# Optimization experiments

Hardware: AMD Instinct MI355X
Metric: run time of the kernel (lower is better)

## Reference

```python
import jax, jax.numpy as jnp
import numpy as np

EPS = 1e-8


def setup_inputs() -> dict:
    key = jax.random.key(0)
    ks = jax.random.split(key, 5)
    B, C, F, T = 2, 8, 1024, 256
    Ch, Fh = 4 * C, 4 * F  # expanded channels/features
    s_pw1 = 1.0 / np.sqrt(F)
    s_dw1 = 1.0 / np.sqrt(C)
    s_pw2 = 1.0 / np.sqrt(Fh)
    s_dw2 = 1.0 / np.sqrt(Ch)
    return {
        "x": jax.random.normal(ks[0], (B, C, F, T), jnp.float32),
        "ln_w": jnp.ones((C, F), jnp.float32),
        "ln_b": jnp.zeros((C, F), jnp.float32),
        "pw1": jax.random.uniform(ks[1], (C, Fh, F), jnp.float32, -s_pw1, s_pw1),
        "dw1": jax.random.uniform(ks[2], (Ch, C), jnp.float32, -s_dw1, s_dw1),
        "pw2": jax.random.uniform(ks[3], (Ch, F, Fh), jnp.float32, -s_pw2, s_pw2),
        "dw2": jax.random.uniform(ks[4], (C, Ch), jnp.float32, -s_dw2, s_dw2),
    }


def _mc_layernorm(x, w, b):
    # x: (B,C,F,T); normalize over feature axis (2), affine per (channel, feature)
    mu = jnp.mean(x, axis=2, keepdims=True)
    var = jnp.var(x, axis=2, keepdims=True)
    xn = (x - mu) * jax.lax.rsqrt(var + EPS)
    return xn * w[None, :, :, None] + b[None, :, :, None]


def reference(x, ln_w, ln_b, pw1, dw1, pw2, dw2):
    h = _mc_layernorm(x, ln_w, ln_b)
    # per-channel positionwise linear: (C, F_out, F_in)
    h = jnp.einsum('bcft,cgf->bcgt', h, pw1)
    # channel mixing (depthwise linear across channels): (C_out, C_in)
    h = jnp.einsum('bcft,dc->bdft', h, dw1)
    h = jnp.square(jax.nn.relu(h))  # squared ReLU
    h = jnp.einsum('bcft,cgf->bcgt', h, pw2)
    h = jnp.einsum('bcft,dc->bdft', h, dw2)
    return x + h
```

## Files before the change

kernel.cpp:

```cpp
#include <hip/hip_runtime.h>

#define B_DIM  2
#define C_DIM  8
#define F_DIM  1024
#define T_DIM  256
#define CH_DIM 32
#define FH_DIM 4096
#define BT_DIM 512

typedef __bf16 bf16x8 __attribute__((ext_vector_type(8)));
typedef __bf16 bf16x4 __attribute__((ext_vector_type(4)));
typedef float  f32x4  __attribute__((ext_vector_type(4)));

__device__ __forceinline__ void async16(const void* g, void* l) {
  __builtin_amdgcn_global_load_lds(
      (const __attribute__((address_space(1))) unsigned int*)g,
      (__attribute__((address_space(3))) unsigned int*)l, 16, 0, 0);
}

#define LGKM0_SCHED() do { \
    asm volatile("s_waitcnt lgkmcnt(0)" ::: "memory"); \
    __builtin_amdgcn_sched_barrier(0); } while (0)

__global__ void ln_kernel(const float* __restrict__ x,
                          const float* __restrict__ lnw,
                          const float* __restrict__ lnb,
                          __bf16* __restrict__ hn) {
  const int tb = blockIdx.x;
  const int c  = blockIdx.y;
  const int b  = blockIdx.z;
  const int tid = threadIdx.x;
  const int tx = tid & 15, ty = tid >> 4;
  const int t0 = tb * 16;

  const float* xp = x + (size_t)(b * C_DIM + c) * F_DIM * T_DIM;

  float s = 0.f, s2 = 0.f;
  for (int f = ty; f < F_DIM; f += 16) {
    float v = xp[f * T_DIM + t0 + tx];
    s += v; s2 += v * v;
  }
  __shared__ float ps[16][16], ps2[16][16];
  __shared__ float mean_s[16], rstd_s[16];
  ps[ty][tx] = s; ps2[ty][tx] = s2;
  __syncthreads();
  if (tid < 16) {
    float a = 0.f, a2 = 0.f;
    for (int j = 0; j < 16; ++j) { a += ps[j][tid]; a2 += ps2[j][tid]; }
    float mu  = a * (1.0f / F_DIM);
    float var = a2 * (1.0f / F_DIM) - mu * mu;
    mean_s[tid] = mu;
    rstd_s[tid] = rsqrtf(var + 1e-8f);
  }
  __syncthreads();

  __shared__ float tile[64][17];
  __bf16* hp = hn + ((size_t)c * BT_DIM + b * T_DIM + t0) * F_DIM;
  for (int ff = 0; ff < 16; ++ff) {
    const int f0 = ff * 64;
#pragma unroll
    for (int it = 0; it < 4; ++it) {
      int e  = it * 256 + tid;
      int fi = e >> 4, ti = e & 15;
      float v = xp[(f0 + fi) * T_DIM + t0 + ti];
      v = (v - mean_s[ti]) * rstd_s[ti];
      v = v * lnw[c * F_DIM + f0 + fi] + lnb[c * F_DIM + f0 + fi];
      tile[fi][ti] = v;
    }
    __syncthreads();
#pragma unroll
    for (int it = 0; it < 4; ++it) {
      int e  = it * 256 + tid;
      int fx = e & 63, tw = e >> 6;
      hp[(size_t)tw * F_DIM + f0 + fx] = (__bf16)tile[fx][tw];
    }
    __syncthreads();
  }
}

template<int TPB_BITS, bool CT>
__global__ __launch_bounds__(512, 2)
void gemm_8p(const float* __restrict__ A, const __bf16* __restrict__ Bm,
             __bf16* __restrict__ Co, const int M, const int K) {
  const int NT = K >> 6;
  const int bid = blockIdx.x;
  const int xcd = bid & 7, idx = bid >> 3;
  const int batch = xcd * (32 >> TPB_BITS) + (idx >> TPB_BITS);
  const int tile  = idx & ((1 << TPB_BITS) - 1);
  const int mt = tile >> 1, nt = tile & 1;

  const int tid = threadIdx.x, lane = tid & 63, wid = tid >> 6;

  const float*  Ab = A  + (size_t)batch * M * K + (size_t)(mt * 256) * K;
  const __bf16* Bb = Bm + (size_t)batch * BT_DIM * K + (size_t)(nt * 256) * K;

  extern __shared__ __align__(16) char smem[];
  __bf16* const AS = (__bf16*)smem;
  __bf16* const BS = (__bf16*)(smem + 65536);

  const int wm = wid >> 2, wn = wid & 3;
  const int lr = lane & 15, khi = lane >> 4;
  const int lsw = lr & 7;

  const int b_row = lane >> 3;
  const int b_src = (lane & 7) ^ b_row;

  f32x4 acc[8][4] = {};
  float4 sa[8];
  bf16x8 af[4];

  auto issueB1 = [&](int sbuf, int tt, int j) {
    const int chunk = j * 8 + wid;
    async16(Bb + (size_t)(chunk * 8 + b_row) * K + (size_t)tt * 64 + b_src * 8,
            BS + sbuf * 16384 + chunk * 512);
  };
  auto issueA2 = [&](int tt, int i0) {
#pragma unroll
    for (int i = i0; i < i0 + 2; ++i) {
      const int c = i * 512 + tid;
      sa[i] = *(const float4*)(Ab + (size_t)(c >> 4) * K + (size_t)tt * 64 + (c & 15) * 4);
    }
  };
  auto writeA2 = [&](int abuf, int i0) {
#pragma unroll
    for (int i = i0; i < i0 + 2; ++i) {
      const int c = i * 512 + tid;
      const int r = c >> 4;
      const int s = ((c & 15) >> 1) ^ (r & 7);
      bf16x4 v;
      v[0]=(__bf16)sa[i].x; v[1]=(__bf16)sa[i].y; v[2]=(__bf16)sa[i].z; v[3]=(__bf16)sa[i].w;
      *(bf16x4*)(AS + abuf * 16384 + r * 64 + s * 8 + (c & 1) * 4) = v;
    }
  };
  auto readA = [&](int abuf, int mq, int ks) {
#pragma unroll
    for (int j = 0; j < 4; ++j) {
      const int row = wm * 128 + (mq * 4 + j) * 16 + lr;
      af[j] = *(const bf16x8*)(AS + abuf * 16384 + row * 64 + (((ks << 2) | khi) ^ lsw) * 8);
    }
  };
  auto readB2 = [&](bf16x8* bq, int rbuf, int np, int ks) {
#pragma unroll
    for (int j = 0; j < 2; ++j) {
      const int row = wn * 64 + (np * 2 + j) * 16 + lr;
      bq[j] = *(const bf16x8*)(BS + rbuf * 16384 + row * 64 + (((ks << 2) | khi) ^ lsw) * 8);
    }
  };
  auto mfma8 = [&](const bf16x8* bq, int mq, int np) {
    __builtin_amdgcn_s_setprio(1);
#pragma unroll
    for (int j = 0; j < 4; ++j)
#pragma unroll
      for (int n = 0; n < 2; ++n)
        acc[mq * 4 + j][np * 2 + n] =
            __builtin_amdgcn_mfma_f32_16x16x32_bf16(af[j], bq[n], acc[mq * 4 + j][np * 2 + n], 0, 0, 0);
    __builtin_amdgcn_s_setprio(0);
  };

  issueA2(0, 0); issueA2(0, 2); issueA2(0, 4); issueA2(0, 6);
  issueB1(0, 0, 0); issueB1(0, 0, 1); issueB1(0, 0, 2); issueB1(0, 0, 3);
  issueB1(1, 1, 0); issueB1(1, 1, 1); issueB1(1, 1, 2); issueB1(1, 1, 3);
  writeA2(0, 0); writeA2(0, 2); writeA2(0, 4); writeA2(0, 6);
  issueA2(1, 0); issueA2(1, 2); issueA2(1, 4); issueA2(1, 6);
  asm volatile("s_waitcnt vmcnt(12)" ::: "memory");
  LGKM0_SCHED();
  __builtin_amdgcn_s_barrier();

  int cur = 0;
  for (int t = 0; t < NT; ++t) {
    const int rd = t % 3, st = (t + 2) % 3;
    const int tN = (t + 2 < NT) ? t + 2 : NT - 1;
    bf16x8 bq[2];
    issueB1(st, tN, 0);
    readA(cur, 0, 0); readB2(bq, rd, 0, 0);
    __builtin_amdgcn_s_barrier(); LGKM0_SCHED();
    mfma8(bq, 0, 0); __builtin_amdgcn_s_barrier();
    issueB1(st, tN, 1);
    readB2(bq, rd, 1, 0);
    __builtin_amdgcn_s_barrier(); LGKM0_SCHED();
    mfma8(bq, 0, 1); __builtin_amdgcn_s_barrier();
    issueB1(st, tN, 2);
    readA(cur, 1, 0); readB2(bq, rd, 0, 0);
    __builtin_amdgcn_s_barrier(); LGKM0_SCHED();
    mfma8(bq, 1, 0); __builtin_amdgcn_s_barrier();
    issueB1(st, tN, 3);
    readB2(bq, rd, 1, 0);
    __builtin_amdgcn_s_barrier(); LGKM0_SCHED();
    mfma8(bq, 1, 1); __builtin_amdgcn_s_barrier();
    writeA2(cur ^ 1, 0); issueA2(tN, 0);
    readA(cur, 0, 1); readB2(bq, rd, 0, 1);
    __builtin_amdgcn_s_barrier(); LGKM0_SCHED();
    mfma8(bq, 0, 0); __builtin_amdgcn_s_barrier();
    writeA2(cur ^ 1, 2); issueA2(tN, 2);
    readB2(bq, rd, 1, 1);
    __builtin_amdgcn_s_barrier(); LGKM0_SCHED();
    mfma8(bq, 0, 1); __builtin_amdgcn_s_barrier();
    writeA2(cur ^ 1, 4); issueA2(tN, 4);
    readA(cur, 1, 1); readB2(bq, rd, 0, 1);
    __builtin_amdgcn_s_barrier(); LGKM0_SCHED();
    mfma8(bq, 1, 0); __builtin_amdgcn_s_barrier();
    writeA2(cur ^ 1, 6); issueA2(tN, 6);
    readB2(bq, rd, 1, 1);
    __builtin_amdgcn_s_barrier(); LGKM0_SCHED();
    mfma8(bq, 1, 1);
    __builtin_amdgcn_s_barrier();
    cur ^= 1;
  }

  const int colc = lane & 15;
  const int rowb = (lane >> 4) * 4;
  if (CT) {
    __bf16* T = (__bf16*)smem + wid * 1152;
#pragma unroll
    for (int h = 0; h < 2; ++h) {
      const int mbase = mt * 256 + wm * 128 + h * 64;
#pragma unroll
      for (int ni = 0; ni < 4; ++ni) {
#pragma unroll
        for (int mi = 0; mi < 4; ++mi)
#pragma unroll
          for (int r = 0; r < 4; ++r)
            T[colc * 72 + mi * 16 + rowb + r] = (__bf16)acc[h * 4 + mi][ni][r];
        __bf16* outp = Co + (size_t)batch * BT_DIM * M
                          + (size_t)(nt * 256 + wn * 64 + ni * 16) * M + mbase + lane;
#pragma unroll
        for (int r16 = 0; r16 < 16; ++r16)
          outp[(size_t)r16 * M] = T[r16 * 72 + lane];
      }
    }
  } else {
#pragma unroll
    for (int mi = 0; mi < 8; ++mi) {
#pragma unroll
      for (int ni = 0; ni < 4; ++ni) {
        const int m = mt * 256 + wm * 128 + mi * 16 + rowb;
        const int n = nt * 256 + wn * 64 + ni * 16 + colc;
#pragma unroll
        for (int r = 0; r < 4; ++r)
          Co[((size_t)batch * M + m + r) * BT_DIM + n] = (__bf16)acc[mi][ni][r];
      }
    }
  }
}

__global__ void mix1_kernel(const __bf16* __restrict__ Y1,
                            const float* __restrict__ dw1,
                            __bf16* __restrict__ h2) {
  const int gidx = blockIdx.x * 256 + threadIdx.x;
  const int g8 = gidx & 511, bt = gidx >> 9;
  const int g0 = g8 * 8;

  float y[C_DIM][8];
#pragma unroll
  for (int c = 0; c < C_DIM; ++c) {
    bf16x8 v = *(const bf16x8*)(Y1 + ((size_t)c * BT_DIM + bt) * FH_DIM + g0);
#pragma unroll
    for (int j = 0; j < 8; ++j) y[c][j] = (float)v[j];
  }
  for (int d = 0; d < CH_DIM; ++d) {
    float s[8] = {0.f,0.f,0.f,0.f,0.f,0.f,0.f,0.f};
#pragma unroll
    for (int c = 0; c < C_DIM; ++c) {
      const float wv = dw1[d * C_DIM + c];
#pragma unroll
      for (int j = 0; j < 8; ++j) s[j] += wv * y[c][j];
    }
    bf16x8 o;
#pragma unroll
    for (int j = 0; j < 8; ++j) {
      float r = s[j] > 0.f ? s[j] : 0.f;
      o[j] = (__bf16)(r * r);
    }
    *(bf16x8*)(h2 + ((size_t)d * BT_DIM + bt) * FH_DIM + g0) = o;
  }
}

__global__ void mix2_kernel(const float* __restrict__ x,
                            const __bf16* __restrict__ Y2,
                            const float* __restrict__ dw2,
                            float* __restrict__ out) {
  const int gidx = blockIdx.x * 256 + threadIdx.x;
  const int t4 = gidx & 63;
  const int f  = (gidx >> 6) & 1023;
  const int b  = gidx >> 16;
  const int t0 = t4 * 4;

  float4 r[C_DIM];
#pragma unroll
  for (int dd = 0; dd < C_DIM; ++dd)
    r[dd] = *(const float4*)(x + ((size_t)(b * C_DIM + dd) * F_DIM + f) * T_DIM + t0);

  for (int d = 0; d < CH_DIM; ++d) {
    bf16x4 v = *(const bf16x4*)(Y2 + ((size_t)d * F_DIM + f) * BT_DIM + b * T_DIM + t0);
    const float v0 = (float)v[0], v1 = (float)v[1], v2 = (float)v[2], v3 = (float)v[3];
#pragma unroll
    for (int dd = 0; dd < C_DIM; ++dd) {
      const float w = dw2[dd * CH_DIM + d];
      r[dd].x += w * v0; r[dd].y += w * v1; r[dd].z += w * v2; r[dd].w += w * v3;
    }
  }
#pragma unroll
  for (int dd = 0; dd < C_DIM; ++dd)
    *(float4*)(out + ((size_t)(b * C_DIM + dd) * F_DIM + f) * T_DIM + t0) = r[dd];
}

extern "C" void kernel_launch(void* const* d_in, const int* in_sizes, int n_in,
                              void* d_out, int out_size, void* d_ws, size_t ws_size,
                              hipStream_t stream) {
  const float* x   = (const float*)d_in[0];
  const float* lnw = (const float*)d_in[1];
  const float* lnb = (const float*)d_in[2];
  const float* pw1 = (const float*)d_in[3];
  const float* dw1 = (const float*)d_in[4];
  const float* pw2 = (const float*)d_in[5];
  const float* dw2 = (const float*)d_in[6];
  float* out = (float*)d_out;

  char* ws = (char*)d_ws;
  __bf16* hn = (__bf16*)(ws);
  __bf16* Y1 = (__bf16*)(ws + (8ULL << 20));
  __bf16* h2 = (__bf16*)(ws + (40ULL << 20));
  __bf16* Y2 = (__bf16*)(ws);

  (void)hipFuncSetAttribute((const void*)gemm_8p<5, true>,
                            hipFuncAttributeMaxDynamicSharedMemorySize, 163840);
  (void)hipFuncSetAttribute((const void*)gemm_8p<3, false>,
                            hipFuncAttributeMaxDynamicSharedMemorySize, 163840);

  ln_kernel<<<dim3(T_DIM / 16, C_DIM, B_DIM), 256, 0, stream>>>(x, lnw, lnb, hn);
  gemm_8p<5, true><<<256, 512, 163840, stream>>>(pw1, hn, Y1, FH_DIM, F_DIM);
  mix1_kernel<<<(BT_DIM * (FH_DIM / 8)) / 256, 256, 0, stream>>>(Y1, dw1, h2);
  gemm_8p<3, false><<<256, 512, 163840, stream>>>(pw2, h2, Y2, F_DIM, FH_DIM);
  mix2_kernel<<<512, 256, 0, stream>>>(x, Y2, dw2, out);
}
```

Measured before the change: 316.7 us.

## Retile GEMM to 128x512 blocks with double-buffered B and per-iteration wait

The GEMM tile changes from 256x256 (M split in two, N split in two) to 128 rows of M by the full 512 columns of N. The B operand pipeline drops from triple to double buffering, and an explicit vmcnt wait is added at the end of each k-step. Each block now covers all of N, so A is read once per batch instead of twice, at the cost of streaming the full B panel per M tile. The per-thread accumulator count is unchanged. The shallower B prefetch may expose more global latency. Launch-side changes to the template parameter and grid are not visible here.

```diff
diff --git a/kernel.cpp b/kernel.cpp
--- a/kernel.cpp
+++ b/kernel.cpp
@@ -78,25 +78,24 @@
   }
 }
 
-template<int TPB_BITS, bool CT>
+template<int MTBITS, bool CT>
 __global__ __launch_bounds__(512, 2)
 void gemm_8p(const float* __restrict__ A, const __bf16* __restrict__ Bm,
              __bf16* __restrict__ Co, const int M, const int K) {
   const int NT = K >> 6;
   const int bid = blockIdx.x;
   const int xcd = bid & 7, idx = bid >> 3;
-  const int batch = xcd * (32 >> TPB_BITS) + (idx >> TPB_BITS);
-  const int tile  = idx & ((1 << TPB_BITS) - 1);
-  const int mt = tile >> 1, nt = tile & 1;
+  const int batch = xcd * (32 >> MTBITS) + (idx >> MTBITS);
+  const int mt    = idx & ((1 << MTBITS) - 1);
 
   const int tid = threadIdx.x, lane = tid & 63, wid = tid >> 6;
 
-  const float*  Ab = A  + (size_t)batch * M * K + (size_t)(mt * 256) * K;
-  const __bf16* Bb = Bm + (size_t)batch * BT_DIM * K + (size_t)(nt * 256) * K;
+  const float*  Ab = A  + (size_t)batch * M * K + (size_t)(mt * 128) * K;
+  const __bf16* Bb = Bm + (size_t)batch * BT_DIM * K;
 
   extern __shared__ __align__(16) char smem[];
   __bf16* const AS = (__bf16*)smem;
-  __bf16* const BS = (__bf16*)(smem + 65536);
+  __bf16* const BS = (__bf16*)(smem + 32768);
 
   const int wm = wid >> 2, wn = wid & 3;
   const int lr = lane & 15, khi = lane >> 4;
@@ -105,104 +104,102 @@
   const int b_row = lane >> 3;
   const int b_src = (lane & 7) ^ b_row;
 
-  f32x4 acc[8][4] = {};
-  float4 sa[8];
+  f32x4 acc[4][8] = {};
+  float4 sa[4];
   bf16x8 af[4];
 
-  auto issueB1 = [&](int sbuf, int tt, int j) {
-    const int chunk = j * 8 + wid;
-    async16(Bb + (size_t)(chunk * 8 + b_row) * K + (size_t)tt * 64 + b_src * 8,
-            BS + sbuf * 16384 + chunk * 512);
-  };
-  auto issueA2 = [&](int tt, int i0) {
-#pragma unroll
-    for (int i = i0; i < i0 + 2; ++i) {
-      const int c = i * 512 + tid;
-      sa[i] = *(const float4*)(Ab + (size_t)(c >> 4) * K + (size_t)tt * 64 + (c & 15) * 4);
-    }
-  };
-  auto writeA2 = [&](int abuf, int i0) {
-#pragma unroll
-    for (int i = i0; i < i0 + 2; ++i) {
-      const int c = i * 512 + tid;
-      const int r = c >> 4;
-      const int s = ((c & 15) >> 1) ^ (r & 7);
-      bf16x4 v;
-      v[0]=(__bf16)sa[i].x; v[1]=(__bf16)sa[i].y; v[2]=(__bf16)sa[i].z; v[3]=(__bf16)sa[i].w;
-      *(bf16x4*)(AS + abuf * 16384 + r * 64 + s * 8 + (c & 1) * 4) = v;
-    }
-  };
-  auto readA = [&](int abuf, int mq, int ks) {
+  auto issueB2 = [&](int sbuf, int tt, int j0) {
+#pragma unroll
+    for (int j = j0; j < j0 + 2; ++j) {
+      const int chunk = j * 8 + wid;
+      async16(Bb + (size_t)(chunk * 8 + b_row) * K + (size_t)tt * 64 + b_src * 8,
+              BS + sbuf * 32768 + chunk * 512);
+    }
+  };
+  auto issueA1 = [&](int tt, int i) {
+    const int c = i * 512 + tid;
+    sa[i] = *(const float4*)(Ab + (size_t)(c >> 4) * K + (size_t)tt * 64 + (c & 15) * 4);
+  };
+  auto writeA1 = [&](int abuf, int i) {
+    const int c = i * 512 + tid;
+    const int r = c >> 4;
+    const int s = ((c & 15) >> 1) ^ (r & 7);
+    bf16x4 v;
+    v[0]=(__bf16)sa[i].x; v[1]=(__bf16)sa[i].y; v[2]=(__bf16)sa[i].z; v[3]=(__bf16)sa[i].w;
+    *(bf16x4*)(AS + abuf * 8192 + r * 64 + s * 8 + (c & 1) * 4) = v;
+  };
+  auto readA = [&](int abuf, int ks) {
 #pragma unroll
     for (int j = 0; j < 4; ++j) {
-      const int row = wm * 128 + (mq * 4 + j) * 16 + lr;
-      af[j] = *(const bf16x8*)(AS + abuf * 16384 + row * 64 + (((ks << 2) | khi) ^ lsw) * 8);
+      const int row = wm * 64 + j * 16 + lr;
+      af[j] = *(const bf16x8*)(AS + abuf * 8192 + row * 64 + (((ks << 2) | khi) ^ lsw) * 8);
     }
   };
   auto readB2 = [&](bf16x8* bq, int rbuf, int np, int ks) {
 #pragma unroll
     for (int j = 0; j < 2; ++j) {
-      const int row = wn * 64 + (np * 2 + j) * 16 + lr;
-      bq[j] = *(const bf16x8*)(BS + rbuf * 16384 + row * 64 + (((ks << 2) | khi) ^ lsw) * 8);
-    }
-  };
-  auto mfma8 = [&](const bf16x8* bq, int mq, int np) {
+      const int row = wn * 128 + (np * 2 + j) * 16 + lr;
+      bq[j] = *(const bf16x8*)(BS + rbuf * 32768 + row * 64 + (((ks << 2) | khi) ^ lsw) * 8);
+    }
+  };
+  auto mfma8 = [&](const bf16x8* bq, int np) {
     __builtin_amdgcn_s_setprio(1);
 #pragma unroll
     for (int j = 0; j < 4; ++j)
 #pragma unroll
       for (int n = 0; n < 2; ++n)
-        acc[mq * 4 + j][np * 2 + n] =
-            __builtin_amdgcn_mfma_f32_16x16x32_bf16(af[j], bq[n], acc[mq * 4 + j][np * 2 + n], 0, 0, 0);
+        acc[j][np * 2 + n] =
+            __builtin_amdgcn_mfma_f32_16x16x32_bf16(af[j], bq[n], acc[j][np * 2 + n], 0, 0, 0);
     __builtin_amdgcn_s_setprio(0);
   };
 
-  issueA2(0, 0); issueA2(0, 2); issueA2(0, 4); issueA2(0, 6);
-  issueB1(0, 0, 0); issueB1(0, 0, 1); issueB1(0, 0, 2); issueB1(0, 0, 3);
-  issueB1(1, 1, 0); issueB1(1, 1, 1); issueB1(1, 1, 2); issueB1(1, 1, 3);
-  writeA2(0, 0); writeA2(0, 2); writeA2(0, 4); writeA2(0, 6);
-  issueA2(1, 0); issueA2(1, 2); issueA2(1, 4); issueA2(1, 6);
-  asm volatile("s_waitcnt vmcnt(12)" ::: "memory");
+  issueA1(0, 0); issueA1(0, 1); issueA1(0, 2); issueA1(0, 3);
+  issueB2(0, 0, 0); issueB2(0, 0, 2); issueB2(0, 0, 4); issueB2(0, 0, 6);
+  writeA1(0, 0); writeA1(0, 1); writeA1(0, 2); writeA1(0, 3);
+  issueA1(1, 0); issueA1(1, 1); issueA1(1, 2); issueA1(1, 3);
+  asm volatile("s_waitcnt vmcnt(4)" ::: "memory");
   LGKM0_SCHED();
   __builtin_amdgcn_s_barrier();
 
   int cur = 0;
   for (int t = 0; t < NT; ++t) {
-    const int rd = t % 3, st = (t + 2) % 3;
-    const int tN = (t + 2 < NT) ? t + 2 : NT - 1;
+    const int tB = (t + 1 < NT) ? t + 1 : NT - 1;
+    const int tA = (t + 2 < NT) ? t + 2 : NT - 1;
     bf16x8 bq[2];
-    issueB1(st, tN, 0);
-    readA(cur, 0, 0); readB2(bq, rd, 0, 0);
-    __builtin_amdgcn_s_barrier(); LGKM0_SCHED();
-    mfma8(bq, 0, 0); __builtin_amdgcn_s_barrier();
-    issueB1(st, tN, 1);
-    readB2(bq, rd, 1, 0);
-    __builtin_amdgcn_s_barrier(); LGKM0_SCHED();
-    mfma8(bq, 0, 1); __builtin_amdgcn_s_barrier();
-    issueB1(st, tN, 2);
-    readA(cur, 1, 0); readB2(bq, rd, 0, 0);
-    __builtin_amdgcn_s_barrier(); LGKM0_SCHED();
-    mfma8(bq, 1, 0); __builtin_amdgcn_s_barrier();
-    issueB1(st, tN, 3);
-    readB2(bq, rd, 1, 0);
-    __builtin_amdgcn_s_barrier(); LGKM0_SCHED();
-    mfma8(bq, 1, 1); __builtin_amdgcn_s_barrier();
-    writeA2(cur ^ 1, 0); issueA2(tN, 0);
-    readA(cur, 0, 1); readB2(bq, rd, 0, 1);
-    __builtin_amdgcn_s_barrier(); LGKM0_SCHED();
-    mfma8(bq, 0, 0); __builtin_amdgcn_s_barrier();
-    writeA2(cur ^ 1, 2); issueA2(tN, 2);
-    readB2(bq, rd, 1, 1);
-    __builtin_amdgcn_s_barrier(); LGKM0_SCHED();
-    mfma8(bq, 0, 1); __builtin_amdgcn_s_barrier();
-    writeA2(cur ^ 1, 4); issueA2(tN, 4);
-    readA(cur, 1, 1); readB2(bq, rd, 0, 1);
-    __builtin_amdgcn_s_barrier(); LGKM0_SCHED();
-    mfma8(bq, 1, 0); __builtin_amdgcn_s_barrier();
-    writeA2(cur ^ 1, 6); issueA2(tN, 6);
-    readB2(bq, rd, 1, 1);
-    __builtin_amdgcn_s_barrier(); LGKM0_SCHED();
-    mfma8(bq, 1, 1);
+    issueB2(cur ^ 1, tB, 0);
+    readA(cur, 0); readB2(bq, cur, 0, 0);
+    __builtin_amdgcn_s_barrier(); LGKM0_SCHED();
+    mfma8(bq, 0); __builtin_amdgcn_s_barrier();
+    issueB2(cur ^ 1, tB, 2);
+    readB2(bq, cur, 1, 0);
+    __builtin_amdgcn_s_barrier(); LGKM0_SCHED();
+    mfma8(bq, 1); __builtin_amdgcn_s_barrier();
+    issueB2(cur ^ 1, tB, 4);
+    readB2(bq, cur, 2, 0);
+    __builtin_amdgcn_s_barrier(); LGKM0_SCHED();
+    mfma8(bq, 2); __builtin_amdgcn_s_barrier();
+    issueB2(cur ^ 1, tB, 6);
+    readB2(bq, cur, 3, 0);
+    __builtin_amdgcn_s_barrier(); LGKM0_SCHED();
+    mfma8(bq, 3); __builtin_amdgcn_s_barrier();
+    writeA1(cur ^ 1, 0); issueA1(tA, 0);
+    readA(cur, 1); readB2(bq, cur, 0, 1);
+    __builtin_amdgcn_s_barrier(); LGKM0_SCHED();
+    mfma8(bq, 0); __builtin_amdgcn_s_barrier();
+    writeA1(cur ^ 1, 1); issueA1(tA, 1);
+    readB2(bq, cur, 1, 1);
+    __builtin_amdgcn_s_barrier(); LGKM0_SCHED();
+    mfma8(bq, 1); __builtin_amdgcn_s_barrier();
+    writeA1(cur ^ 1, 2); issueA1(tA, 2);
+    readB2(bq, cur, 2, 1);
+    __builtin_amdgcn_s_barrier(); LGKM0_SCHED();
+    mfma8(bq, 2); __builtin_amdgcn_s_barrier();
+    writeA1(cur ^ 1, 3); issueA1(tA, 3);
+    readB2(bq, cur, 3, 1);
+    __builtin_amdgcn_s_barrier(); LGKM0_SCHED();
+    mfma8(bq, 3);
+    asm volatile("s_waitcnt vmcnt(4)" ::: "memory");
+    LGKM0_SCHED();
     __builtin_amdgcn_s_barrier();
     cur ^= 1;
   }
@@ -211,30 +208,27 @@
   const int rowb = (lane >> 4) * 4;
   if (CT) {
     __bf16* T = (__bf16*)smem + wid * 1152;
-#pragma unroll
-    for (int h = 0; h < 2; ++h) {
-      const int mbase = mt * 256 + wm * 128 + h * 64;
-#pragma unroll
-      for (int ni = 0; ni < 4; ++ni) {
-#pragma unroll
-        for (int mi = 0; mi < 4; ++mi)
-#pragma unroll
-          for (int r = 0; r < 4; ++r)
-            T[colc * 72 + mi * 16 + rowb + r] = (__bf16)acc[h * 4 + mi][ni][r];
-        __bf16* outp = Co + (size_t)batch * BT_DIM * M
-                          + (size_t)(nt * 256 + wn * 64 + ni * 16) * M + mbase + lane;
-#pragma unroll
-        for (int r16 = 0; r16 < 16; ++r16)
-          outp[(size_t)r16 * M] = T[r16 * 72 + lane];
-      }
+    const int mbase = mt * 128 + wm * 64;
+#pragma unroll
+    for (int ni = 0; ni < 8; ++ni) {
+#pragma unroll
+      for (int mi = 0; mi < 4; ++mi)
+#pragma unroll
+        for (int r = 0; r < 4; ++r)
+          T[colc * 72 + mi * 16 + rowb + r] = (__bf16)acc[mi][ni][r];
+      __bf16* outp = Co + (size_t)batch * BT_DIM * M
+                        + (size_t)(wn * 128 + ni * 16) * M + mbase + lane;
+#pragma unroll
+      for (int r16 = 0; r16 < 16; ++r16)
+        outp[(size_t)r16 * M] = T[r16 * 72 + lane];
     }
   } else {
 #pragma unroll
-    for (int mi = 0; mi < 8; ++mi) {
-#pragma unroll
-      for (int ni = 0; ni < 4; ++ni) {
-        const int m = mt * 256 + wm * 128 + mi * 16 + rowb;
-        const int n = nt * 256 + wn * 64 + ni * 16 + colc;
+    for (int mi = 0; mi < 4; ++mi) {
+#pragma unroll
+      for (int ni = 0; ni < 8; ++ni) {
+        const int m = mt * 128 + wm * 64 + mi * 16 + rowb;
+        const int n = wn * 128 + ni * 16 + colc;
 #pragma unroll
         for (int r = 0; r < 4; ++r)
           Co[((size_t)batch * M + m + r) * BT_DIM + n] = (__bf16)acc[mi][ni][r];
```

Measured after the change: 330.3 us. 4.3% more time.
